# Optimization experiments

Hardware: AMD Instinct MI355X
Metric: run time of the kernel (lower is better)

## Reference

```python
import jax, jax.numpy as jnp
import numpy as np

B, S, D, H = 2, 2048, 1024, 16
HD = D // H

def setup_inputs() -> dict:
    key = jax.random.key(0)
    ks = jax.random.split(key, 11)
    s = 1.0 / np.sqrt(D)
    return {
        "query": jax.random.normal(ks[0], (B, S, D), jnp.float32),
        "key": jax.random.normal(ks[1], (B, S, D), jnp.float32),
        "value": jax.random.normal(ks[2], (B, S, D), jnp.float32),
        "Wq": jax.random.normal(ks[3], (D, D), jnp.float32) * s,
        "bq": jax.random.normal(ks[4], (D,), jnp.float32) * s,
        "Wk": jax.random.normal(ks[5], (D, D), jnp.float32) * s,
        "bk": jax.random.normal(ks[6], (D,), jnp.float32) * s,
        "Wv": jax.random.normal(ks[7], (D, D), jnp.float32) * s,
        "bv": jax.random.normal(ks[8], (D,), jnp.float32) * s,
        "Wo": jax.random.normal(ks[9], (D, D), jnp.float32) * s,
        "bo": jax.random.normal(ks[10], (D,), jnp.float32) * s,
        "test": 0,
    }

def _heads(x, W, b):
    # [B,S,D] @ [D,D] -> [B,S,D] -> [B,H,S,HD]
    y = x @ W + b
    return y.reshape(B, -1, H, HD).transpose(0, 2, 1, 3)

def reference(query, key, value, Wq, bq, Wk, bk, Wv, bv, Wo, bo, test):
    q = _heads(query, Wq, bq)
    k = _heads(key, Wk, bk)
    v = _heads(value, Wv, bv)
    scale = 1.0 / np.sqrt(HD).astype(np.float32)
    scores = jnp.einsum('bhqd,bhkd->bhqk', q, k) * scale  # [B,H,S,S]
    if test:
        return scores
    prob = jax.nn.softmax(scores, axis=-1)
    out = jnp.einsum('bhqk,bhkd->bhqd', prob, v)
    out = out.transpose(0, 2, 1, 3).reshape(B, -1, D)
    return out @ Wo + bo
```

## Files before the change

kernel.cpp:

```cpp
#include <hip/hip_runtime.h>

constexpr int Bn  = 2;
constexpr int Sn  = 2048;
constexpr int Dn  = 1024;
constexpr int Hn  = 16;
constexpr int HDn = 64;
constexpr int Mn  = Bn * Sn;

typedef _Float16 half8 __attribute__((ext_vector_type(8)));
typedef _Float16 half4 __attribute__((ext_vector_type(4)));
typedef float    f32x4 __attribute__((ext_vector_type(4)));

__device__ __forceinline__ void cp16(const _Float16* g, _Float16* l) {
  __builtin_amdgcn_global_load_lds(
      (__attribute__((address_space(1))) void*)g,
      (__attribute__((address_space(3))) void*)l, 16, 0, 0);
}

__global__ __launch_bounds__(256) void prep_kernel(
    const float* __restrict__ q, const float* __restrict__ k,
    const float* __restrict__ v,
    const float* __restrict__ Wq, const float* __restrict__ Wk,
    const float* __restrict__ Wv, const float* __restrict__ Wo,
    _Float16* __restrict__ Xh, _Float16* __restrict__ WT) {
  __shared__ float tile[64][65];
  const int n = blockIdx.x;
  const int tid = threadIdx.x;
  if (n < 12288) {
    const int z = n >> 12;
    const float* src = (z == 0) ? q : (z == 1) ? k : v;
    _Float16* dst = Xh + (size_t)z * (Mn * Dn);
    int i = (n & 4095) * 256 + tid;
    float4 v4 = ((const float4*)src)[i];
    half4 h;
    h.x = (_Float16)v4.x; h.y = (_Float16)v4.y;
    h.z = (_Float16)v4.z; h.w = (_Float16)v4.w;
    *(half4*)(dst + (size_t)i * 4) = h;
  } else {
    const int m = n - 12288;
    const int z = m >> 8, rem = m & 255;
    const float* W = (z == 0) ? Wq : (z == 1) ? Wk : (z == 2) ? Wv : Wo;
    _Float16* T = WT + (size_t)z * Dn * Dn;
    const int k0 = (rem >> 4) * 64, n0 = (rem & 15) * 64;
#pragma unroll
    for (int i = 0; i < 4; i++) {
      int s = tid + i * 256;
      int r = s >> 4, c4 = s & 15;
      float4 w4 = *(const float4*)(W + (size_t)(k0 + r) * Dn + n0 + c4 * 4);
      tile[r][c4 * 4 + 0] = w4.x; tile[r][c4 * 4 + 1] = w4.y;
      tile[r][c4 * 4 + 2] = w4.z; tile[r][c4 * 4 + 3] = w4.w;
    }
    __syncthreads();
#pragma unroll
    for (int i = 0; i < 2; i++) {
      int s = tid + i * 256;
      int nn = s >> 3, r8 = (s & 7) * 8;
      half8 h;
#pragma unroll
      for (int j = 0; j < 8; j++) h[j] = (_Float16)tile[r8 + j][nn];
      *(half8*)(T + (size_t)(n0 + nn) * Dn + k0 + r8) = h;
    }
  }
}

__global__ __launch_bounds__(256) void proj_kernel(
    const _Float16* __restrict__ Xh, const _Float16* __restrict__ WT,
    const float* __restrict__ bq, const float* __restrict__ bk,
    const float* __restrict__ bv,
    _Float16* __restrict__ Qh, _Float16* __restrict__ Kh,
    _Float16* __restrict__ VT) {
  const int z = blockIdx.z;
  const _Float16* A  = Xh + (size_t)z * Mn * Dn;
  const _Float16* Bm = WT + (size_t)z * Dn * Dn;
  const float* bias = (z == 0) ? bq : (z == 1) ? bk : bv;

  __shared__ __align__(16) _Float16 smem[2 * 128 * 64];
  _Float16* As = smem;
  _Float16* Bs = smem + 128 * 64;

  const int tid  = threadIdx.x;
  const int lane = tid & 63;
  const int w    = tid >> 6;
  const int wm   = (w >> 1) * 64;
  const int wn   = (w & 1) * 64;
  const int m0   = blockIdx.y * 128;
  const int n0   = blockIdx.x * 128;
  const int qd   = lane >> 4;
  const int lm   = lane & 15;

  const int st_r = tid >> 3;
  const int st_u = (tid & 7) ^ (st_r & 7);

  f32x4 acc[4][4];
#pragma unroll
  for (int i = 0; i < 4; i++)
#pragma unroll
    for (int j = 0; j < 4; j++) acc[i][j] = {0.f, 0.f, 0.f, 0.f};

  for (int k0 = 0; k0 < Dn; k0 += 64) {
#pragma unroll
    for (int p = 0; p < 4; p++) {
      int row = st_r + p * 32;
      cp16(A + (size_t)(m0 + row) * Dn + k0 + st_u * 8, As + (tid + p * 256) * 8);
      cp16(Bm + (size_t)(n0 + row) * Dn + k0 + st_u * 8, Bs + (tid + p * 256) * 8);
    }
    __syncthreads();
#pragma unroll
    for (int ks = 0; ks < 2; ks++) {
      const int up = ((ks * 4 + qd) ^ (lm & 7)) * 8;
      half8 a[4], bb[4];
#pragma unroll
      for (int mi = 0; mi < 4; mi++)
        a[mi] = *(const half8*)(As + (wm + mi * 16 + lm) * 64 + up);
#pragma unroll
      for (int ni = 0; ni < 4; ni++)
        bb[ni] = *(const half8*)(Bs + (wn + ni * 16 + lm) * 64 + up);
      if (z < 2) {
#pragma unroll
        for (int mi = 0; mi < 4; mi++)
#pragma unroll
          for (int ni = 0; ni < 4; ni++)
            acc[mi][ni] = __builtin_amdgcn_mfma_f32_16x16x32_f16(bb[ni], a[mi], acc[mi][ni], 0, 0, 0);
      } else {
#pragma unroll
        for (int mi = 0; mi < 4; mi++)
#pragma unroll
          for (int ni = 0; ni < 4; ni++)
            acc[mi][ni] = __builtin_amdgcn_mfma_f32_16x16x32_f16(a[mi], bb[ni], acc[mi][ni], 0, 0, 0);
      }
    }
    __syncthreads();
  }

  char* T = (char*)smem;
  const int b_ = m0 >> 11, s0 = m0 & (Sn - 1), h0 = n0 >> 6;

  if (z < 2) {
    _Float16* out = (z == 0) ? Qh : Kh;
    const float scl = (z == 0) ? 0.125f * 1.44269504089f : 1.0f;
#pragma unroll
    for (int mi = 0; mi < 4; mi++) {
      int tok = wm + mi * 16 + lm;
#pragma unroll
      for (int ni = 0; ni < 4; ni++) {
        int feat = wn + ni * 16 + qd * 4;
        float4 b4 = *(const float4*)(bias + n0 + feat);
        half4 h4;
        h4[0] = (_Float16)((acc[mi][ni][0] + b4.x) * scl);
        h4[1] = (_Float16)((acc[mi][ni][1] + b4.y) * scl);
        h4[2] = (_Float16)((acc[mi][ni][2] + b4.z) * scl);
        h4[3] = (_Float16)((acc[mi][ni][3] + b4.w) * scl);
        *(half4*)(T + tok * 256 + ((feat * 2) ^ ((tok & 7) << 4))) = h4;
      }
    }
    __syncthreads();
#pragma unroll
    for (int i = 0; i < 8; i++) {
      int slot = tid + i * 256;
      int r = slot >> 3, c16 = slot & 7;
      int hh = r >> 7, sm = r & 127;
      half8 v8 = *(const half8*)(T + sm * 256 + ((hh * 128 + c16 * 16) ^ ((sm & 7) << 4)));
      *(half8*)(out + (((size_t)(b_ * Hn + h0 + hh)) * Sn + s0 + sm) * HDn + c16 * 8) = v8;
    }
  } else {
#pragma unroll
    for (int ni = 0; ni < 4; ni++) {
      int feat = wn + ni * 16 + lm;
      float b_f = bias[n0 + feat];
#pragma unroll
      for (int mi = 0; mi < 4; mi++) {
        int tk = wm + mi * 16 + qd * 4;
        half4 h4;
#pragma unroll
        for (int r = 0; r < 4; r++) h4[r] = (_Float16)(acc[mi][ni][r] + b_f);
        *(half4*)(T + feat * 256 + ((tk * 2) ^ ((feat & 7) << 4))) = h4;
      }
    }
    __syncthreads();
#pragma unroll
    for (int i = 0; i < 8; i++) {
      int slot = tid + i * 256;
      int f = slot >> 4, c16 = slot & 15;
      half8 v8 = *(const half8*)(T + f * 256 + ((c16 * 16) ^ ((f & 7) << 4)));
      int head = h0 + (f >> 6), hd = f & 63;
      *(half8*)(VT + (((size_t)(b_ * Hn + head)) * HDn + hd) * Sn + s0 + c16 * 8) = v8;
    }
  }
}

__global__ __launch_bounds__(256, 3) void attn_kernel(
    const _Float16* __restrict__ Qh, const _Float16* __restrict__ Kh,
    const _Float16* __restrict__ VT, _Float16* __restrict__ attn_out) {
  constexpr int PV_LD = 72;
  __shared__ __align__(16) _Float16 Ksb[2][128 * 64];
  __shared__ __align__(16) _Float16 Ps[4 * 32 * PV_LD];

  const int n    = blockIdx.x;
  const int slot = n >> 3;
  const int bh   = (n & 7) * 4 + (slot >> 4);
  const int q0   = (slot & 15) * 128;
  const size_t base = (size_t)bh * Sn * HDn;

  const int tid  = threadIdx.x;
  const int lane = tid & 63;
  const int w    = tid >> 6;
  const int qd   = lane >> 4;
  const int lm   = lane & 15;

  const _Float16* qptr = Qh + base + (size_t)(q0 + w * 32 + lm) * HDn + qd * 8;
  half8 qa[2][2];
#pragma unroll
  for (int nj = 0; nj < 2; nj++)
#pragma unroll
    for (int ks = 0; ks < 2; ks++)
      qa[nj][ks] = *(const half8*)(qptr + nj * 16 * HDn + ks * 32);

  half8 vones;
#pragma unroll
  for (int j = 0; j < 8; j++) vones[j] = (lm == 0) ? (_Float16)1.0f : (_Float16)0.0f;

  f32x4 oacc[2][4];
#pragma unroll
  for (int i = 0; i < 2; i++)
#pragma unroll
    for (int j = 0; j < 4; j++) oacc[i][j] = {0.f, 0.f, 0.f, 0.f};
  f32x4 oaccl[2] = {{0.f, 0.f, 0.f, 0.f}, {0.f, 0.f, 0.f, 0.f}};

  _Float16* Psw = Ps + w * (32 * PV_LD);
  const f32x4 sinit = {-10.f, -10.f, -10.f, -10.f};

  const int st_r = tid >> 3;
  const int st_u = (tid & 7) ^ (st_r & 7);
  const _Float16* kbase = Kh + base;

#define STAGE_K(KT, DST)                                                     \
  {                                                                          \
    const _Float16* src_ = kbase + (size_t)(KT) * 128 * HDn;                 \
    _Float16* dst_ = (DST);                                                  \
    _Pragma("unroll")                                                        \
    for (int p = 0; p < 4; p++)                                              \
      cp16(src_ + (size_t)(st_r + p * 32) * HDn + st_u * 8,                  \
           dst_ + (tid + p * 256) * 8);                                      \
  }

  STAGE_K(0, Ksb[0])
  __syncthreads();

  int cur = 0;
  for (int kt = 0; kt < Sn / 128; kt++) {
    const int kb = kt * 128;
    if (kt + 1 < Sn / 128) STAGE_K(kt + 1, Ksb[cur ^ 1])

#pragma unroll
    for (int c = 0; c < 2; c++) {
      f32x4 sacc[4][2];
#pragma unroll
      for (int n4 = 0; n4 < 4; n4++)
#pragma unroll
        for (int nj = 0; nj < 2; nj++) sacc[n4][nj] = sinit;
      __builtin_amdgcn_s_setprio(1);
#pragma unroll
      for (int n4 = 0; n4 < 4; n4++) {
        int ni = 4 * c + n4;
#pragma unroll
        for (int ks = 0; ks < 2; ks++) {
          int up = (4 * ks + qd) ^ (lm & 7);
          half8 ka = *(const half8*)(Ksb[cur] + (ni * 16 + lm) * HDn + up * 8);
#pragma unroll
          for (int nj = 0; nj < 2; nj++)
            sacc[n4][nj] = __builtin_amdgcn_mfma_f32_16x16x32_f16(ka, qa[nj][ks], sacc[n4][nj], 0, 0, 0);
        }
      }
      __builtin_amdgcn_s_setprio(0);

      half8 vb[4][2];
#pragma unroll
      for (int oi = 0; oi < 4; oi++)
#pragma unroll
        for (int k2 = 0; k2 < 2; k2++)
          vb[oi][k2] = *(const half8*)(VT + base + (size_t)(oi * 16 + lm) * Sn
                                       + kb + c * 64 + k2 * 32 + qd * 8);

#pragma unroll
      for (int nj = 0; nj < 2; nj++)
#pragma unroll
        for (int n4 = 0; n4 < 4; n4++) {
          float p0 = __builtin_amdgcn_exp2f(sacc[n4][nj][0]);
          float p1 = __builtin_amdgcn_exp2f(sacc[n4][nj][1]);
          float p2 = __builtin_amdgcn_exp2f(sacc[n4][nj][2]);
          float p3 = __builtin_amdgcn_exp2f(sacc[n4][nj][3]);
          auto lo = __builtin_amdgcn_cvt_pkrtz(p0, p1);
          auto hi = __builtin_amdgcn_cvt_pkrtz(p2, p3);
          half4 h4;
          h4[0] = (_Float16)lo[0]; h4[1] = (_Float16)lo[1];
          h4[2] = (_Float16)hi[0]; h4[3] = (_Float16)hi[1];
          *(half4*)(Psw + (nj * 16 + lm) * PV_LD + n4 * 16 + qd * 4) = h4;
        }

#pragma unroll
      for (int k2 = 0; k2 < 2; k2++) {
        half8 pa[2];
#pragma unroll
        for (int mi = 0; mi < 2; mi++)
          pa[mi] = *(const half8*)(Psw + (mi * 16 + lm) * PV_LD + k2 * 32 + qd * 8);
        __builtin_amdgcn_s_setprio(1);
#pragma unroll
        for (int oi = 0; oi < 4; oi++)
#pragma unroll
          for (int mi = 0; mi < 2; mi++)
            oacc[mi][oi] = __builtin_amdgcn_mfma_f32_16x16x32_f16(vb[oi][k2], pa[mi], oacc[mi][oi], 0, 0, 0);
#pragma unroll
        for (int mi = 0; mi < 2; mi++)
          oaccl[mi] = __builtin_amdgcn_mfma_f32_16x16x32_f16(vones, pa[mi], oaccl[mi], 0, 0, 0);
        __builtin_amdgcn_s_setprio(0);
      }
    }

    __syncthreads();
    cur ^= 1;
  }
#undef STAGE_K

  const int b_ = bh >> 4, h_ = bh & 15;
#pragma unroll
  for (int mi = 0; mi < 2; mi++) {
    float lr = __shfl(oaccl[mi][0], lm, 64);
    float inv = 1.0f / lr;
    int qrow = q0 + w * 32 + mi * 16 + lm;
    size_t rowbase = ((size_t)(b_ * Sn + qrow)) * Dn + h_ * 64;
#pragma unroll
    for (int oi = 0; oi < 4; oi++) {
      half4 h4;
#pragma unroll
      for (int r = 0; r < 4; r++) h4[r] = (_Float16)(oacc[mi][oi][r] * inv);
      *(half4*)(attn_out + rowbase + oi * 16 + qd * 4) = h4;
    }
  }
}

__global__ __launch_bounds__(256) void outproj_kernel(
    const _Float16* __restrict__ Aattn, const _Float16* __restrict__ WoT,
    const float* __restrict__ bo, float* __restrict__ out) {
  __shared__ __align__(16) _Float16 smem[(64 + 128) * 128];
  _Float16* As = smem;
  _Float16* Bs = smem + 64 * 128;

  const int tid  = threadIdx.x;
  const int lane = tid & 63;
  const int w    = tid >> 6;
  const int wm   = (w >> 1) * 32;
  const int wn   = (w & 1) * 64;
  const int m0   = blockIdx.y * 64;
  const int n0   = blockIdx.x * 128;
  const int qd   = lane >> 4;
  const int lm   = lane & 15;

  f32x4 acc[2][4];
#pragma unroll
  for (int i = 0; i < 2; i++)
#pragma unroll
    for (int j = 0; j < 4; j++) acc[i][j] = {0.f, 0.f, 0.f, 0.f};

  for (int k0 = 0; k0 < Dn; k0 += 128) {
#pragma unroll
    for (int p = 0; p < 4; p++) {
      int s = tid + p * 256;
      int r = s >> 4, u = (s & 15) ^ (r & 15);
      cp16(Aattn + (size_t)(m0 + r) * Dn + k0 + u * 8, As + s * 8);
    }
#pragma unroll
    for (int p = 0; p < 8; p++) {
      int s = tid + p * 256;
      int r = s >> 4, u = (s & 15) ^ (r & 15);
      cp16(WoT + (size_t)(n0 + r) * Dn + k0 + u * 8, Bs + s * 8);
    }
    __syncthreads();
#pragma unroll
    for (int ks = 0; ks < 4; ks++) {
      const int up = (ks * 4 + qd) ^ lm;
      half8 a[2], bb[4];
#pragma unroll
      for (int mi = 0; mi < 2; mi++)
        a[mi] = *(const half8*)(As + ((wm + mi * 16 + lm) * 16 + up) * 8);
#pragma unroll
      for (int ni = 0; ni < 4; ni++)
        bb[ni] = *(const half8*)(Bs + ((wn + ni * 16 + lm) * 16 + up) * 8);
#pragma unroll
      for (int mi = 0; mi < 2; mi++)
#pragma unroll
        for (int ni = 0; ni < 4; ni++)
          acc[mi][ni] = __builtin_amdgcn_mfma_f32_16x16x32_f16(bb[ni], a[mi], acc[mi][ni], 0, 0, 0);
    }
    __syncthreads();
  }

  float* T = (float*)smem;
#pragma unroll
  for (int mi = 0; mi < 2; mi++) {
    int m = wm + mi * 16 + lm;
#pragma unroll
    for (int ni = 0; ni < 4; ni++) {
      int nb = wn + ni * 16 + qd * 4;
      float4 b4 = *(const float4*)(bo + n0 + nb);
      f32x4 o;
      o[0] = acc[mi][ni][0] + b4.x;
      o[1] = acc[mi][ni][1] + b4.y;
      o[2] = acc[mi][ni][2] + b4.z;
      o[3] = acc[mi][ni][3] + b4.w;
      *(f32x4*)((char*)T + m * 512 + ((nb * 4) ^ ((m & 7) << 4))) = o;
    }
  }
  __syncthreads();
#pragma unroll
  for (int i = 0; i < 8; i++) {
    int s = tid + i * 256;
    int r = s >> 5, c = s & 31;
    f32x4 v = *(const f32x4*)((char*)T + r * 512 + ((c * 16) ^ ((r & 7) << 4)));
    *(f32x4*)(out + (size_t)(m0 + r) * Dn + n0 + c * 4) = v;
  }
}

extern "C" void kernel_launch(void* const* d_in, const int* in_sizes, int n_in,
                              void* d_out, int out_size, void* d_ws, size_t ws_size,
                              hipStream_t stream) {
  const float* query = (const float*)d_in[0];
  const float* key_  = (const float*)d_in[1];
  const float* value = (const float*)d_in[2];
  const float* Wq = (const float*)d_in[3];
  const float* bq = (const float*)d_in[4];
  const float* Wk = (const float*)d_in[5];
  const float* bk = (const float*)d_in[6];
  const float* Wv = (const float*)d_in[7];
  const float* bv = (const float*)d_in[8];
  const float* Wo = (const float*)d_in[9];
  const float* bo = (const float*)d_in[10];

  _Float16* Xh = (_Float16*)d_ws;
  _Float16* WT = Xh + (size_t)3 * Mn * Dn;
  _Float16* Qh = WT + (size_t)4 * Dn * Dn;
  _Float16* Kh = Qh + (size_t)Mn * Dn;
  _Float16* VT = Kh + (size_t)Mn * Dn;
  _Float16* attnb = Xh;
  float* out = (float*)d_out;

  dim3 blk(256);
  prep_kernel<<<dim3(12288 + 1024), blk, 0, stream>>>(
      query, key_, value, Wq, Wk, Wv, Wo, Xh, WT);
  proj_kernel<<<dim3(Dn / 128, Mn / 128, 3), blk, 0, stream>>>(
      Xh, WT, bq, bk, bv, Qh, Kh, VT);
  attn_kernel<<<dim3(512), blk, 0, stream>>>(Qh, Kh, VT, attnb);
  outproj_kernel<<<dim3(Dn / 128, Mn / 64), blk, 0, stream>>>(
      attnb, WT + (size_t)3 * Dn * Dn, bo, out);
}
```

Before: 245.6 us.

## Software-pipeline QK, softmax and PV across the two key sub-chunks in attention

Restructures the per-tile attention loop so both QK^T sub-chunk MFMAs are issued before the softmax/PV stages. V loads are hoisted earlier and double-buffered so global latency overlaps with MFMA work. To fit the extra live score accumulators and V registers, the occupancy hint drops from 3 to 2 waves-groups per SIMD. The trade-off is higher register pressure and less latency hiding through occupancy.

Result: no change. 241.4 us (-1.7%).

```diff
diff --git a/kernel.cpp b/kernel.cpp
--- a/kernel.cpp
+++ b/kernel.cpp
@@ -188,7 +188,7 @@
   }
 }
 
-__global__ __launch_bounds__(256, 3) void attn_kernel(
+__global__ __launch_bounds__(256, 2) void attn_kernel(
     const _Float16* __restrict__ Qh, const _Float16* __restrict__ Kh,
     const _Float16* __restrict__ VT, _Float16* __restrict__ attn_out) {
   constexpr int PV_LD = 72;
@@ -232,6 +232,7 @@
   const int st_r = tid >> 3;
   const int st_u = (tid & 7) ^ (st_r & 7);
   const _Float16* kbase = Kh + base;
+  const _Float16* vrow  = VT + base + (size_t)lm * Sn + qd * 8;
 
 #define STAGE_K(KT, DST)                                                     \
   {                                                                          \
@@ -243,6 +244,75 @@
            dst_ + (tid + p * 256) * 8);                                      \
   }
 
+#define LOAD_V(C, VB)                                                        \
+  _Pragma("unroll")                                                          \
+  for (int oi = 0; oi < 4; oi++)                                             \
+    _Pragma("unroll")                                                        \
+    for (int k2 = 0; k2 < 2; k2++)                                           \
+      VB[oi][k2] = *(const half8*)(vrow + (size_t)(oi * 16) * Sn             \
+                                   + kb + (C) * 64 + k2 * 32);
+
+#define QK(C, SACC)                                                          \
+  {                                                                          \
+    _Pragma("unroll")                                                        \
+    for (int n4 = 0; n4 < 4; n4++)                                           \
+      _Pragma("unroll")                                                      \
+      for (int nj = 0; nj < 2; nj++) SACC[n4][nj] = sinit;                   \
+    __builtin_amdgcn_s_setprio(1);                                           \
+    _Pragma("unroll")                                                        \
+    for (int n4 = 0; n4 < 4; n4++) {                                         \
+      int ni = 4 * (C) + n4;                                                 \
+      _Pragma("unroll")                                                      \
+      for (int ks = 0; ks < 2; ks++) {                                       \
+        int up = (4 * ks + qd) ^ (lm & 7);                                   \
+        half8 ka = *(const half8*)(Ksb[cur] + (ni * 16 + lm) * HDn + up * 8);\
+        _Pragma("unroll")                                                    \
+        for (int nj = 0; nj < 2; nj++)                                       \
+          SACC[n4][nj] = __builtin_amdgcn_mfma_f32_16x16x32_f16(             \
+              ka, qa[nj][ks], SACC[n4][nj], 0, 0, 0);                        \
+      }                                                                      \
+    }                                                                        \
+    __builtin_amdgcn_s_setprio(0);                                           \
+  }
+
+#define SM(SACC)                                                             \
+  _Pragma("unroll")                                                          \
+  for (int nj = 0; nj < 2; nj++)                                             \
+    _Pragma("unroll")                                                        \
+    for (int n4 = 0; n4 < 4; n4++) {                                         \
+      float p0 = __builtin_amdgcn_exp2f(SACC[n4][nj][0]);                    \
+      float p1 = __builtin_amdgcn_exp2f(SACC[n4][nj][1]);                    \
+      float p2 = __builtin_amdgcn_exp2f(SACC[n4][nj][2]);                    \
+      float p3 = __builtin_amdgcn_exp2f(SACC[n4][nj][3]);                    \
+      auto lo = __builtin_amdgcn_cvt_pkrtz(p0, p1);                          \
+      auto hi = __builtin_amdgcn_cvt_pkrtz(p2, p3);                          \
+      half4 h4;                                                              \
+      h4[0] = (_Float16)lo[0]; h4[1] = (_Float16)lo[1];                      \
+      h4[2] = (_Float16)hi[0]; h4[3] = (_Float16)hi[1];                      \
+      *(half4*)(Psw + (nj * 16 + lm) * PV_LD + n4 * 16 + qd * 4) = h4;       \
+    }
+
+#define PV(VB)                                                               \
+  _Pragma("unroll")                                                          \
+  for (int k2 = 0; k2 < 2; k2++) {                                           \
+    half8 pa[2];                                                             \
+    _Pragma("unroll")                                                        \
+    for (int mi = 0; mi < 2; mi++)                                           \
+      pa[mi] = *(const half8*)(Psw + (mi * 16 + lm) * PV_LD + k2 * 32 + qd * 8);\
+    __builtin_amdgcn_s_setprio(1);                                           \
+    _Pragma("unroll")                                                        \
+    for (int oi = 0; oi < 4; oi++)                                           \
+      _Pragma("unroll")                                                      \
+      for (int mi = 0; mi < 2; mi++)                                         \
+        oacc[mi][oi] = __builtin_amdgcn_mfma_f32_16x16x32_f16(               \
+            VB[oi][k2], pa[mi], oacc[mi][oi], 0, 0, 0);                      \
+    _Pragma("unroll")                                                        \
+    for (int mi = 0; mi < 2; mi++)                                           \
+      oaccl[mi] = __builtin_amdgcn_mfma_f32_16x16x32_f16(                    \
+          vones, pa[mi], oaccl[mi], 0, 0, 0);                                \
+    __builtin_amdgcn_s_setprio(0);                                           \
+  }
+
   STAGE_K(0, Ksb[0])
   __syncthreads();
 
@@ -251,75 +321,26 @@
     const int kb = kt * 128;
     if (kt + 1 < Sn / 128) STAGE_K(kt + 1, Ksb[cur ^ 1])
 
-#pragma unroll
-    for (int c = 0; c < 2; c++) {
-      f32x4 sacc[4][2];
-#pragma unroll
-      for (int n4 = 0; n4 < 4; n4++)
-#pragma unroll
-        for (int nj = 0; nj < 2; nj++) sacc[n4][nj] = sinit;
-      __builtin_amdgcn_s_setprio(1);
-#pragma unroll
-      for (int n4 = 0; n4 < 4; n4++) {
-        int ni = 4 * c + n4;
-#pragma unroll
-        for (int ks = 0; ks < 2; ks++) {
-          int up = (4 * ks + qd) ^ (lm & 7);
-          half8 ka = *(const half8*)(Ksb[cur] + (ni * 16 + lm) * HDn + up * 8);
-#pragma unroll
-          for (int nj = 0; nj < 2; nj++)
-            sacc[n4][nj] = __builtin_amdgcn_mfma_f32_16x16x32_f16(ka, qa[nj][ks], sacc[n4][nj], 0, 0, 0);
-        }
-      }
-      __builtin_amdgcn_s_setprio(0);
-
-      half8 vb[4][2];
-#pragma unroll
-      for (int oi = 0; oi < 4; oi++)
-#pragma unroll
-        for (int k2 = 0; k2 < 2; k2++)
-          vb[oi][k2] = *(const half8*)(VT + base + (size_t)(oi * 16 + lm) * Sn
-                                       + kb + c * 64 + k2 * 32 + qd * 8);
-
-#pragma unroll
-      for (int nj = 0; nj < 2; nj++)
-#pragma unroll
-        for (int n4 = 0; n4 < 4; n4++) {
-          float p0 = __builtin_amdgcn_exp2f(sacc[n4][nj][0]);
-          float p1 = __builtin_amdgcn_exp2f(sacc[n4][nj][1]);
-          float p2 = __builtin_amdgcn_exp2f(sacc[n4][nj][2]);
-          float p3 = __builtin_amdgcn_exp2f(sacc[n4][nj][3]);
-          auto lo = __builtin_amdgcn_cvt_pkrtz(p0, p1);
-          auto hi = __builtin_amdgcn_cvt_pkrtz(p2, p3);
-          half4 h4;
-          h4[0] = (_Float16)lo[0]; h4[1] = (_Float16)lo[1];
-          h4[2] = (_Float16)hi[0]; h4[3] = (_Float16)hi[1];
-          *(half4*)(Psw + (nj * 16 + lm) * PV_LD + n4 * 16 + qd * 4) = h4;
-        }
-
-#pragma unroll
-      for (int k2 = 0; k2 < 2; k2++) {
-        half8 pa[2];
-#pragma unroll
-        for (int mi = 0; mi < 2; mi++)
-          pa[mi] = *(const half8*)(Psw + (mi * 16 + lm) * PV_LD + k2 * 32 + qd * 8);
-        __builtin_amdgcn_s_setprio(1);
-#pragma unroll
-        for (int oi = 0; oi < 4; oi++)
-#pragma unroll
-          for (int mi = 0; mi < 2; mi++)
-            oacc[mi][oi] = __builtin_amdgcn_mfma_f32_16x16x32_f16(vb[oi][k2], pa[mi], oacc[mi][oi], 0, 0, 0);
-#pragma unroll
-        for (int mi = 0; mi < 2; mi++)
-          oaccl[mi] = __builtin_amdgcn_mfma_f32_16x16x32_f16(vones, pa[mi], oaccl[mi], 0, 0, 0);
-        __builtin_amdgcn_s_setprio(0);
-      }
-    }
+    f32x4 sacc[2][4][2];
+    half8 vbA[4][2], vbB[4][2];
+
+    LOAD_V(0, vbA)
+    QK(0, sacc[0])
+    QK(1, sacc[1])
+    SM(sacc[0])
+    LOAD_V(1, vbB)
+    PV(vbA)
+    SM(sacc[1])
+    PV(vbB)
 
     __syncthreads();
     cur ^= 1;
   }
 #undef STAGE_K
+#undef LOAD_V
+#undef QK
+#undef SM
+#undef PV
 
   const int b_ = bh >> 4, h_ = bh & 15;
 #pragma unroll
```
